# Kernel optimization log

Hardware: AMD Instinct MI355X
Metric: run time of the kernel (lower is better)

The kernel has to match this reference:

```python
import jax, jax.numpy as jnp
import numpy as np

VOCAB, DIM = 100000, 512
BATCH, SEQ = 4096, 200
HID, OUT = 256, 20


def setup_inputs() -> dict:
    key = jax.random.key(0)
    k_emb, k_x, k_len, k_w1, k_b1, k_w2, k_b2 = jax.random.split(key, 7)
    emb_table = jax.random.normal(k_emb, (VOCAB, DIM), dtype=jnp.float32) * 0.1
    x = jax.random.randint(k_x, (BATCH, SEQ), 0, VOCAB, dtype=jnp.int64)
    # lengths in [1, SEQ] to avoid division by zero, matching real padded batches
    lengths = jax.random.randint(k_len, (BATCH,), 1, SEQ + 1, dtype=jnp.int64)
    bows = jnp.zeros((BATCH,), dtype=jnp.float32)  # unused by the model's forward
    # Linear(2*DIM, 256) and Linear(256, OUT); stored transposed for x @ W
    W1 = jax.random.normal(k_w1, (2 * DIM, HID), dtype=jnp.float32) * (1.0 / np.sqrt(2 * DIM))
    b1 = jax.random.normal(k_b1, (HID,), dtype=jnp.float32) * 0.01
    W2 = jax.random.normal(k_w2, (HID, OUT), dtype=jnp.float32) * (1.0 / np.sqrt(HID))
    b2 = jax.random.normal(k_b2, (OUT,), dtype=jnp.float32) * 0.01
    return {"emb_table": emb_table, "W1": W1, "b1": b1, "W2": W2, "b2": b2,
            "x": x, "lengths": lengths, "bows": bows}


def reference(emb_table, W1, b1, W2, b2, x, lengths, bows):
    # Gather: [B, S, D]
    emb = emb_table[x]
    # Faithful to original: sum over the FULL sequence (padding included),
    # divided by the true length; max also over the full sequence.
    rep_mean = jnp.sum(emb, axis=1) / lengths.astype(emb.dtype)[:, None]  # [B, D]
    rep_max = jnp.max(emb, axis=1)                                        # [B, D]
    rep = jnp.concatenate([rep_mean, rep_max], axis=1)                    # [B, 2D]
    h = jax.nn.relu(rep @ W1 + b1)                                        # [B, 256]
    logits = h @ W2 + b2                                                  # [B, OUT]
    return logits
```

## Files before the change

### kernel.cpp

```cpp
#include <hip/hip_runtime.h>
#include <hip/hip_bf16.h>

#define VOCAB 100000
#define DIM   512
#define BATCH 4096
#define SEQ   200
#define HID   256
#define OUTN  20

typedef __attribute__((ext_vector_type(8))) short short8;
typedef __attribute__((ext_vector_type(4))) float floatx4;

static __device__ __forceinline__ unsigned short f2bf(float f) {
    __hip_bfloat16 b = __float2bfloat16(f);
    return *(unsigned short*)&b;
}

__global__ __launch_bounds__(128) void k_reduce(
    const float* __restrict__ emb, const int* __restrict__ x,
    const int* __restrict__ lengths, unsigned short* __restrict__ repb)
{
    const int b = blockIdx.x;
    const int t = threadIdx.x;

    __shared__ int sidx[SEQ];
    for (int i = t; i < SEQ; i += 128) sidx[i] = x[b * SEQ + i];
    __syncthreads();

    const float4* embv = (const float4*)emb;
    float4 s = make_float4(0.f, 0.f, 0.f, 0.f);
    float4 m = make_float4(-1e30f, -1e30f, -1e30f, -1e30f);

#pragma unroll 4
    for (int i = 0; i < SEQ; ++i) {
        const float4 v = embv[(size_t)sidx[i] * (DIM / 4) + t];
        s.x += v.x; s.y += v.y; s.z += v.z; s.w += v.w;
        m.x = fmaxf(m.x, v.x); m.y = fmaxf(m.y, v.y);
        m.z = fmaxf(m.z, v.z); m.w = fmaxf(m.w, v.w);
    }

    const float inv = 1.0f / (float)lengths[b];

    unsigned long long mu =
          (unsigned long long)f2bf(s.x * inv)
        | ((unsigned long long)f2bf(s.y * inv) << 16)
        | ((unsigned long long)f2bf(s.z * inv) << 32)
        | ((unsigned long long)f2bf(s.w * inv) << 48);
    unsigned long long xu =
          (unsigned long long)f2bf(m.x)
        | ((unsigned long long)f2bf(m.y) << 16)
        | ((unsigned long long)f2bf(m.z) << 32)
        | ((unsigned long long)f2bf(m.w) << 48);

    unsigned short* row = repb + (size_t)b * (2 * DIM);
    *(unsigned long long*)(row + 4 * t)       = mu;
    *(unsigned long long*)(row + DIM + 4 * t) = xu;
}

__global__ __launch_bounds__(256) void k_w1t(
    const float* __restrict__ W1, unsigned short* __restrict__ W1T)
{
    __shared__ unsigned short s[64][65];
    const int n0 = blockIdx.x * 64;
    const int k0 = blockIdx.y * 64;
    const int t = threadIdx.x;

#pragma unroll
    for (int i = 0; i < 4; ++i) {
        const int kk = (t >> 4) + i * 16;
        const int cc = (t & 15) * 4;
        const float4 v = *(const float4*)&W1[(size_t)(k0 + kk) * HID + n0 + cc];
        s[cc + 0][kk] = f2bf(v.x);
        s[cc + 1][kk] = f2bf(v.y);
        s[cc + 2][kk] = f2bf(v.z);
        s[cc + 3][kk] = f2bf(v.w);
    }
    __syncthreads();

#pragma unroll
    for (int i = 0; i < 4; ++i) {
        const int nn = (t >> 4) + i * 16;
        const int kq = (t & 15) * 4;
        unsigned long long u =
              (unsigned long long)s[nn][kq + 0]
            | ((unsigned long long)s[nn][kq + 1] << 16)
            | ((unsigned long long)s[nn][kq + 2] << 32)
            | ((unsigned long long)s[nn][kq + 3] << 48);
        *(unsigned long long*)&W1T[(size_t)(n0 + nn) * (2 * DIM) + k0 + kq] = u;
    }
}

__global__ __launch_bounds__(256) void k_gemm1(
    const unsigned short* __restrict__ repb,
    const unsigned short* __restrict__ w1t,
    const float* __restrict__ bias, float* __restrict__ h)
{
    const int K = 2 * DIM;
    const int rowBase = blockIdx.y * 64;
    const int colBase = blockIdx.x * 64;
    const int tid  = threadIdx.x;
    const int lane = tid & 63;
    const int wv   = tid >> 6;
    const int wm   = wv & 1;
    const int wn   = wv >> 1;

    __shared__ unsigned short sA[64][32];
    __shared__ unsigned short sB[64][32];

    const int r  = tid >> 2;
    const int kq = tid & 3;

    const unsigned short* gA = repb + (size_t)(rowBase + r) * K + kq * 8;
    const unsigned short* gB = w1t  + (size_t)(colBase + r) * K + kq * 8;

    floatx4 acc[2][2] = {{{0.f,0.f,0.f,0.f},{0.f,0.f,0.f,0.f}},
                         {{0.f,0.f,0.f,0.f},{0.f,0.f,0.f,0.f}}};

    short8 pa = *(const short8*)gA;
    short8 pb = *(const short8*)gB;

    const int lm = lane & 15;
    const int lq = lane >> 4;
    for (int k0 = 0; k0 < K; k0 += 32) {
        __syncthreads();
        *(short8*)&sA[r][kq * 8] = pa;
        *(short8*)&sB[r][kq * 8] = pb;
        __syncthreads();

        if (k0 + 32 < K) {
            pa = *(const short8*)(gA + k0 + 32);
            pb = *(const short8*)(gB + k0 + 32);
        }

        const short8 a0 = *(const short8*)&sA[wm * 32 + lm][lq * 8];
        const short8 a1 = *(const short8*)&sA[wm * 32 + 16 + lm][lq * 8];
        const short8 b0 = *(const short8*)&sB[wn * 32 + lm][lq * 8];
        const short8 b1 = *(const short8*)&sB[wn * 32 + 16 + lm][lq * 8];

        acc[0][0] = __builtin_amdgcn_mfma_f32_16x16x32_bf16(a0, b0, acc[0][0], 0, 0, 0);
        acc[0][1] = __builtin_amdgcn_mfma_f32_16x16x32_bf16(a0, b1, acc[0][1], 0, 0, 0);
        acc[1][0] = __builtin_amdgcn_mfma_f32_16x16x32_bf16(a1, b0, acc[1][0], 0, 0, 0);
        acc[1][1] = __builtin_amdgcn_mfma_f32_16x16x32_bf16(a1, b1, acc[1][1], 0, 0, 0);
    }

#pragma unroll
    for (int nt = 0; nt < 2; ++nt) {
        const int col = colBase + wn * 32 + nt * 16 + lm;
        const float bb = bias[col];
#pragma unroll
        for (int mt = 0; mt < 2; ++mt) {
#pragma unroll
            for (int rg = 0; rg < 4; ++rg) {
                const int row = rowBase + wm * 32 + mt * 16 + lq * 4 + rg;
                h[(size_t)row * HID + col] = fmaxf(acc[mt][nt][rg] + bb, 0.f);
            }
        }
    }
}

#define R3 32
#define HPAD 260

__global__ __launch_bounds__(256) void k_gemm2(
    const float* __restrict__ H, const float* __restrict__ W2,
    const float* __restrict__ b2, float* __restrict__ outp)
{
    __shared__ float sh[R3 * HPAD];
    __shared__ float sw[HID * OUTN];
    __shared__ float sb[OUTN];

    const int t = threadIdx.x;
    const int rowBase = blockIdx.x * R3;

    const float4* H4 = (const float4*)H;
    for (int i = t; i < R3 * (HID / 4); i += 256) {
        const int r  = i >> 6;
        const int c4 = i & 63;
        *(float4*)&sh[r * HPAD + c4 * 4] = H4[(size_t)(rowBase + r) * (HID / 4) + c4];
    }
    for (int i = t; i < HID * OUTN; i += 256) sw[i] = W2[i];
    if (t < OUTN) sb[t] = b2[t];
    __syncthreads();

    for (int o = t; o < R3 * OUTN; o += 256) {
        const int r = o / OUTN;
        const int c = o - r * OUTN;
        float acc = sb[c];
#pragma unroll 8
        for (int k = 0; k < HID; ++k)
            acc += sh[r * HPAD + k] * sw[k * OUTN + c];
        outp[(size_t)(rowBase + r) * OUTN + c] = acc;
    }
}

extern "C" void kernel_launch(void* const* d_in, const int* in_sizes, int n_in,
                              void* d_out, int out_size, void* d_ws, size_t ws_size,
                              hipStream_t stream)
{
    const float* emb     = (const float*)d_in[0];
    const float* W1      = (const float*)d_in[1];
    const float* b1      = (const float*)d_in[2];
    const float* W2      = (const float*)d_in[3];
    const float* b2      = (const float*)d_in[4];
    const int*   x       = (const int*)d_in[5];
    const int*   lengths = (const int*)d_in[6];

    float* out = (float*)d_out;

    unsigned short* repb = (unsigned short*)d_ws;
    unsigned short* w1t  = repb + (size_t)BATCH * 2 * DIM;
    float* h = (float*)(w1t + (size_t)HID * 2 * DIM);

    k_w1t<<<dim3(HID / 64, (2 * DIM) / 64), 256, 0, stream>>>(W1, w1t);
    k_reduce<<<BATCH, 128, 0, stream>>>(emb, x, lengths, repb);
    k_gemm1<<<dim3(HID / 64, BATCH / 64), 256, 0, stream>>>(repb, w1t, b1, h);
    k_gemm2<<<BATCH / R3, 256, 0, stream>>>(h, W2, b2, out);
}
```

Measured before the change: 487.0 us.

## Convert embedding table to bf16 per call and gather bf16 rows

After: 441.9 us. 9.3% less time.

```diff
diff --git a/kernel.cpp b/kernel.cpp
--- a/kernel.cpp
+++ b/kernel.cpp
@@ -15,6 +15,83 @@
     __hip_bfloat16 b = __float2bfloat16(f);
     return *(unsigned short*)&b;
 }
+static __device__ __forceinline__ float bf2f(unsigned short u) {
+    unsigned int v = (unsigned int)u << 16;
+    return *(float*)&v;
+}
+
+__global__ __launch_bounds__(256) void k_cvt(
+    const float* __restrict__ src, unsigned short* __restrict__ dst)
+{
+    const int n8 = VOCAB * DIM / 8;
+    int i = blockIdx.x * 256 + threadIdx.x;
+    const int stride = gridDim.x * 256;
+    const float4* s4 = (const float4*)src;
+    short8* d8 = (short8*)dst;
+    for (; i < n8; i += stride) {
+        const float4 a = s4[2 * i];
+        const float4 b = s4[2 * i + 1];
+        short8 o;
+        o[0] = (short)f2bf(a.x); o[1] = (short)f2bf(a.y);
+        o[2] = (short)f2bf(a.z); o[3] = (short)f2bf(a.w);
+        o[4] = (short)f2bf(b.x); o[5] = (short)f2bf(b.y);
+        o[6] = (short)f2bf(b.z); o[7] = (short)f2bf(b.w);
+        d8[i] = o;
+    }
+}
+
+__global__ __launch_bounds__(128) void k_reduce_bf(
+    const unsigned short* __restrict__ embb, const int* __restrict__ x,
+    const int* __restrict__ lengths, unsigned short* __restrict__ repb)
+{
+    const int b = blockIdx.x;
+    const int t = threadIdx.x;
+    const int w = t >> 6;
+    const int lane = t & 63;
+
+    __shared__ int sidx[SEQ];
+    for (int i = t; i < SEQ; i += 128) sidx[i] = x[b * SEQ + i];
+    __syncthreads();
+
+    float s[8] = {0.f, 0.f, 0.f, 0.f, 0.f, 0.f, 0.f, 0.f};
+    float m[8] = {-1e30f, -1e30f, -1e30f, -1e30f, -1e30f, -1e30f, -1e30f, -1e30f};
+
+    const unsigned short* base = embb + lane * 8;
+    const int i0 = w * (SEQ / 2);
+
+#pragma unroll 4
+    for (int i = i0; i < i0 + SEQ / 2; ++i) {
+        const short8 v = *(const short8*)(base + (size_t)sidx[i] * DIM);
+#pragma unroll
+        for (int j = 0; j < 8; ++j) {
+            const float f = bf2f((unsigned short)v[j]);
+            s[j] += f;
+            m[j] = fmaxf(m[j], f);
+        }
+    }
+
+    __shared__ float red[2][2][DIM];
+#pragma unroll
+    for (int j = 0; j < 8; ++j) {
+        red[w][0][lane * 8 + j] = s[j];
+        red[w][1][lane * 8 + j] = m[j];
+    }
+    __syncthreads();
+
+    const float inv = 1.0f / (float)lengths[b];
+    const int c0 = t * 4;
+    unsigned long long mu = 0, xu = 0;
+#pragma unroll
+    for (int j = 0; j < 4; ++j) {
+        const float sv = red[0][0][c0 + j] + red[1][0][c0 + j];
+        const float mv = fmaxf(red[0][1][c0 + j], red[1][1][c0 + j]);
+        mu |= (unsigned long long)f2bf(sv * inv) << (16 * j);
+        xu |= (unsigned long long)f2bf(mv)       << (16 * j);
+    }
+    unsigned short* row = repb + (size_t)b * (2 * DIM);
+    *(unsigned long long*)(row + c0)       = mu;
+    *(unsigned long long*)(row + DIM + c0) = xu;
+}
 
 __global__ __launch_bounds__(128) void k_reduce(
     const float* __restrict__ emb, const int* __restrict__ x,
@@ -40,7 +117,6 @@
     }
 
     const float inv = 1.0f / (float)lengths[b];
-
     unsigned long long mu =
           (unsigned long long)f2bf(s.x * inv)
         | ((unsigned long long)f2bf(s.y * inv) << 16)
@@ -90,6 +166,8 @@
     }
 }
 
+#define APAD 40
+
 __global__ __launch_bounds__(256) void k_gemm1(
     const unsigned short* __restrict__ repb,
     const unsigned short* __restrict__ w1t,
@@ -104,8 +182,8 @@
     const int wm   = wv & 1;
     const int wn   = wv >> 1;
 
-    __shared__ unsigned short sA[64][32];
-    __shared__ unsigned short sB[64][32];
+    __shared__ unsigned short sA[64][APAD];
+    __shared__ unsigned short sB[64][APAD];
 
     const int r  = tid >> 2;
     const int kq = tid & 3;
@@ -207,12 +285,31 @@
 
     float* out = (float*)d_out;
 
-    unsigned short* repb = (unsigned short*)d_ws;
-    unsigned short* w1t  = repb + (size_t)BATCH * 2 * DIM;
-    float* h = (float*)(w1t + (size_t)HID * 2 * DIM);
-
-    k_w1t<<<dim3(HID / 64, (2 * DIM) / 64), 256, 0, stream>>>(W1, w1t);
-    k_reduce<<<BATCH, 128, 0, stream>>>(emb, x, lengths, repb);
-    k_gemm1<<<dim3(HID / 64, BATCH / 64), 256, 0, stream>>>(repb, w1t, b1, h);
-    k_gemm2<<<BATCH / R3, 256, 0, stream>>>(h, W2, b2, out);
-}
+    const size_t embbN = (size_t)VOCAB * DIM;
+    const size_t repbN = (size_t)BATCH * 2 * DIM;
+    const size_t w1tN  = (size_t)HID * 2 * DIM;
+    const size_t hN    = (size_t)BATCH * HID;
+    const size_t needFast = (embbN + repbN + w1tN) * 2 + hN * 4 + 256;
+
+    if (ws_size >= needFast) {
+        unsigned short* embb = (unsigned short*)d_ws;
+        unsigned short* repb = embb + embbN;
+        unsigned short* w1t  = repb + repbN;
+        float* h = (float*)(w1t + w1tN);
+
+        k_cvt<<<2048, 256, 0, stream>>>(emb, embb);
+        k_w1t<<<dim3(HID / 64, (2 * DIM) / 64), 256, 0, stream>>>(W1, w1t);
+        k_reduce_bf<<<BATCH, 128, 0, stream>>>(embb, x, lengths, repb);
+        k_gemm1<<<dim3(HID / 64, BATCH / 64), 256, 0, stream>>>(repb, w1t, b1, h);
+        k_gemm2<<<BATCH / R3, 256, 0, stream>>>(h, W2, b2, out);
+    } else {
+        unsigned short* repb = (unsigned short*)d_ws;
+        unsigned short* w1t  = repb + repbN;
+        float* h = (float*)(w1t + w1tN);
+
+        k_w1t<<<dim3(HID / 64, (2 * DIM) / 64), 256, 0, stream>>>(W1, w1t);
+        k_reduce<<<BATCH, 128, 0, stream>>>(emb, x, lengths, repb);
+        k_gemm1<<<dim3(HID / 64, BATCH / 64), 256, 0, stream>>>(repb, w1t, b1, h);
+        k_gemm2<<<BATCH / R3, 256, 0, stream>>>(h, W2, b2, out);
+    }
+}
```
